# Kernel tuning notes

Hardware: AMD Instinct MI355X
Metric: run time of the kernel (lower is better)

Reference implementation:

```python
import jax, jax.numpy as jnp
import numpy as np

N = 50000
E = 600000
D_IN = 128
D_HID = 128
D_OUT = 40
BN_EPS = 1e-5


def setup_inputs() -> dict:
    key = jax.random.key(0)
    ks = jax.random.split(key, 16)
    g = lambda k, *s: (jax.random.normal(k, s, jnp.float32) * 0.05)
    return {
        "x": jax.random.normal(ks[0], (N, D_IN), jnp.float32),
        "edge_index": jax.random.randint(ks[1], (2, E), 0, N, dtype=jnp.int64),
        "W0": g(ks[2], D_IN, D_HID), "b0": jnp.zeros((D_HID,), jnp.float32),
        "W1": g(ks[3], D_HID, D_HID), "b1": jnp.zeros((D_HID,), jnp.float32),
        "W2": g(ks[4], D_HID, D_OUT), "b2": jnp.zeros((D_OUT,), jnp.float32),
        "g0": 1.0 + g(ks[5], D_HID), "be0": g(ks[6], D_HID),
        "m0": g(ks[7], D_HID), "v0": 0.5 + jax.random.uniform(ks[8], (D_HID,), jnp.float32),
        "g1": 1.0 + g(ks[9], D_HID), "be1": g(ks[10], D_HID),
        "m1": g(ks[11], D_HID), "v1": 0.5 + jax.random.uniform(ks[12], (D_HID,), jnp.float32),
    }


def reference(x, edge_index, W0, b0, W1, b1, W2, b2,
              g0, be0, m0, v0, g1, be1, m1, v1):
    n = x.shape[0]
    loop = jnp.arange(n, dtype=edge_index.dtype)
    # GCN with self-loops: A_hat = A + I, symmetric normalization
    src = jnp.concatenate([edge_index[0], loop])
    dst = jnp.concatenate([edge_index[1], loop])
    deg = jax.ops.segment_sum(jnp.ones_like(dst, jnp.float32), dst, num_segments=n)
    dinv = jax.lax.rsqrt(jnp.maximum(deg, 1.0))
    norm = dinv[src] * dinv[dst]  # [E+N]

    def conv(h, W, b):
        h = h @ W + b                                   # [N, d_out]
        msg = norm[:, None] * h[src]                    # gather + scale
        return jax.ops.segment_sum(msg, dst, num_segments=n)

    def bn_relu(h, g, be, m, v):
        return jax.nn.relu((h - m) * (g * jax.lax.rsqrt(v + BN_EPS)) + be)

    h = bn_relu(conv(x, W0, b0), g0, be0, m0, v0)
    h = bn_relu(conv(h, W1, b1), g1, be1, m1, v1)
    h = conv(h, W2, b2)
    return jax.nn.log_softmax(h, axis=-1)
```

## Files before the change

kernel.cpp:

```cpp
#include <hip/hip_runtime.h>
#include <math.h>

#define BN_EPS 1e-5f
#define CAP 96

typedef unsigned short ushort_t;
typedef __attribute__((ext_vector_type(8))) short short8;
typedef __attribute__((ext_vector_type(4))) float floatx4;

__device__ inline ushort_t f2b(float f) {
    unsigned u = __float_as_uint(f);
    unsigned r = u + 0x7FFFu + ((u >> 16) & 1u);
    return (ushort_t)(r >> 16);
}
__device__ inline float b2f(ushort_t b) { return __uint_as_float(((unsigned)b) << 16); }
__device__ inline float2 u2f2(unsigned u) {
    return make_float2(b2f((ushort_t)(u & 0xffffu)), b2f((ushort_t)(u >> 16)));
}

__device__ inline void cast_weights(const float* __restrict__ W0, const float* __restrict__ W1,
                                    const float* __restrict__ W2, ushort_t* __restrict__ Wt0,
                                    ushort_t* __restrict__ Wt1, ushort_t* __restrict__ Wt2,
                                    int i) {
    if (i < 16384) {
        int nn = i >> 7, k = i & 127;
        Wt0[i] = f2b(W0[k * 128 + nn]);
    } else if (i < 32768) {
        int j = i - 16384;
        int nn = j >> 7, k = j & 127;
        Wt1[j] = f2b(W1[k * 128 + nn]);
    } else if (i < 40960) {
        int j = i - 32768;
        int nn = j >> 7, k = j & 127;
        Wt2[j] = (nn < 40) ? f2b(W2[k * 40 + nn]) : (ushort_t)0;
    }
}

__global__ __launch_bounds__(256) void k_fill_cast(
    const int* __restrict__ ei, int* __restrict__ cnt, ushort_t* __restrict__ ell,
    const float* __restrict__ W0, const float* __restrict__ W1, const float* __restrict__ W2,
    ushort_t* __restrict__ Wt0, ushort_t* __restrict__ Wt1, ushort_t* __restrict__ Wt2,
    int E, int FB)
{
    int bid = blockIdx.x;
    if (bid < FB) {
        int e = bid * 256 + threadIdx.x;
        if (e < E) {
            int s = ei[e];
            int d = ei[E + e];
            int p = atomicAdd(&cnt[d], 1);
            if (p < CAP) ell[(size_t)d * CAP + p] = (ushort_t)s;
        }
        return;
    }
    cast_weights(W0, W1, W2, Wt0, Wt1, Wt2, (bid - FB) * 256 + threadIdx.x);
}

template<int NT, bool AF32>
__global__ __launch_bounds__(256) void k_gemm(const void* __restrict__ Av,
                                              const ushort_t* __restrict__ Wt,
                                              const float* __restrict__ bias,
                                              const int* __restrict__ cnt,
                                              ushort_t* __restrict__ C,
                                              int M, int ncols) {
    __shared__ ushort_t Ws[NT * 128];
    const int tid = threadIdx.x;
    const int ntiles = (M + 127) >> 7;
    const int wave = tid >> 6, lane = tid & 63;
    const int m = lane & 15, quad = lane >> 4;
    constexpr int CT = NT / 16;
    const int r0 = wave * 32;

    for (int t = blockIdx.x; t < ntiles; t += gridDim.x) {
        const int rbase = t << 7;
#pragma unroll
        for (int p = 0; p < NT / 16; ++p) {
            int cid = p * 256 + tid;
            int nr = cid >> 4, seg = cid & 15;
            *(uint4*)(Ws + nr * 128 + ((seg ^ (nr & 15)) << 3)) =
                *(const uint4*)(Wt + (size_t)cid * 8);
        }
        __syncthreads();

        floatx4 acc[2][CT];
#pragma unroll
        for (int rt = 0; rt < 2; ++rt)
#pragma unroll
            for (int ct = 0; ct < CT; ++ct) acc[rt][ct] = (floatx4){0.f, 0.f, 0.f, 0.f};

        const int ra = rbase + r0 + m;
        const int rb = ra + 16;
        const bool oka = ra < M, okb = rb < M;

#pragma unroll
        for (int ks = 0; ks < 4; ++ks) {
            int ko = ks * 32 + quad * 8;
            short8 a0 = {0, 0, 0, 0, 0, 0, 0, 0}, a1 = a0;
            if (AF32) {
                const float* A32 = (const float*)Av;
                if (oka) {
                    const float* p = A32 + (size_t)ra * 128 + ko;
                    float4 f0 = *(const float4*)p, f1 = *(const float4*)(p + 4);
                    a0[0] = f2b(f0.x); a0[1] = f2b(f0.y); a0[2] = f2b(f0.z); a0[3] = f2b(f0.w);
                    a0[4] = f2b(f1.x); a0[5] = f2b(f1.y); a0[6] = f2b(f1.z); a0[7] = f2b(f1.w);
                }
                if (okb) {
                    const float* p = A32 + (size_t)rb * 128 + ko;
                    float4 f0 = *(const float4*)p, f1 = *(const float4*)(p + 4);
                    a1[0] = f2b(f0.x); a1[1] = f2b(f0.y); a1[2] = f2b(f0.z); a1[3] = f2b(f0.w);
                    a1[4] = f2b(f1.x); a1[5] = f2b(f1.y); a1[6] = f2b(f1.z); a1[7] = f2b(f1.w);
                }
            } else {
                const ushort_t* A16 = (const ushort_t*)Av;
                if (oka) a0 = *(const short8*)(A16 + (size_t)ra * 128 + ko);
                if (okb) a1 = *(const short8*)(A16 + (size_t)rb * 128 + ko);
            }
#pragma unroll
            for (int ct = 0; ct < CT; ++ct) {
                short8 b = *(const short8*)(Ws + (ct * 16 + m) * 128 + (((ks * 4 + quad) ^ m) << 3));
                acc[0][ct] = __builtin_amdgcn_mfma_f32_16x16x32_bf16(a0, b, acc[0][ct], 0, 0, 0);
                acc[1][ct] = __builtin_amdgcn_mfma_f32_16x16x32_bf16(a1, b, acc[1][ct], 0, 0, 0);
            }
        }

        float dsc[2][4];
#pragma unroll
        for (int rt = 0; rt < 2; ++rt)
#pragma unroll
            for (int r = 0; r < 4; ++r) {
                int gr = rbase + r0 + rt * 16 + quad * 4 + r;
                dsc[rt][r] = (gr < M) ? rsqrtf((float)(cnt[gr] + 1)) : 0.f;
            }

        __syncthreads();
        constexpr int SEGN = NT / 8, CMASK = SEGN - 1;
#pragma unroll
        for (int rt = 0; rt < 2; ++rt)
#pragma unroll
            for (int ct = 0; ct < CT; ++ct) {
                int col = ct * 16 + m;
                float bv = (col < ncols) ? bias[col] : 0.f;
                int seg = col >> 3, cl = col & 7;
#pragma unroll
                for (int r = 0; r < 4; ++r) {
                    int row = r0 + rt * 16 + quad * 4 + r;
                    Ws[row * NT + ((seg ^ (row & CMASK)) << 3) + cl] =
                        f2b((acc[rt][ct][r] + bv) * dsc[rt][r]);
                }
            }
        __syncthreads();
        constexpr int CPT = (128 * SEGN) / 256;
#pragma unroll
        for (int p = 0; p < CPT; ++p) {
            int cid = p * 256 + tid;
            int row = cid / SEGN, seg = cid & CMASK;
            int gr = rbase + row;
            if (gr < M)
                *(uint4*)(C + (size_t)gr * NT + seg * 8) =
                    *(const uint4*)(Ws + row * NT + ((seg ^ (row & CMASK)) << 3));
        }
        __syncthreads();
    }
}

template<int NT>
__global__ __launch_bounds__(512) void fused_ag(
    const ushort_t* __restrict__ h,
    const int* __restrict__ cnt,
    const ushort_t* __restrict__ ell,
    const float* __restrict__ g, const float* __restrict__ be,
    const float* __restrict__ mB, const float* __restrict__ v,
    const ushort_t* __restrict__ Wt,
    const float* __restrict__ bias,
    ushort_t* __restrict__ C,
    int M, int ncols)
{
    __shared__ ushort_t As[16 * 128];
    __shared__ ushort_t Ws[NT * 128];
    const int tid = threadIdx.x;
    const int ntiles = (M + 15) >> 4;
    const int wave = tid >> 6, lane = tid & 63;
    const int m = lane & 15, quad = lane >> 4;
    constexpr int CT = NT / 16;
    const unsigned* h2 = (const unsigned*)h;
    unsigned* As2 = (unsigned*)As;

    const int c0 = lane * 2;
    const float s0f = g[c0] * rsqrtf(v[c0] + BN_EPS);
    const float s1f = g[c0 + 1] * rsqrtf(v[c0 + 1] + BN_EPS);
    const float m0v = mB[c0], m1v = mB[c0 + 1], b0v = be[c0], b1v = be[c0 + 1];

    for (int t = blockIdx.x; t < ntiles; t += gridDim.x) {
        const int rbase = t << 4;

        for (int cid = tid; cid < NT * 16; cid += 512) {
            int nr = cid >> 4, seg = cid & 15;
            *(uint4*)(Ws + nr * 128 + ((seg ^ (nr & 15)) << 3)) =
                *(const uint4*)(Wt + (size_t)cid * 8);
        }

#pragma unroll
        for (int rr = 0; rr < 2; ++rr) {
            const int rl = wave * 2 + rr;
            const int gr = rbase + rl;
            unsigned ov = 0;
            if (gr < M) {
                int cd = cnt[gr];
                float dv = rsqrtf((float)(cd + 1));
                float2 hv = u2f2(h2[(size_t)gr * 64 + lane]);
                float ax = hv.x, ay = hv.y;
                int c = min(cd, CAP);
                const uint4* rowv = (const uint4*)(ell + (size_t)gr * CAP);
                int k = 0;
                for (; k + 8 <= c; k += 8) {
                    uint4 iv = rowv[k >> 3];
                    int s[8] = {(int)(iv.x & 0xffffu), (int)(iv.x >> 16),
                                (int)(iv.y & 0xffffu), (int)(iv.y >> 16),
                                (int)(iv.z & 0xffffu), (int)(iv.z >> 16),
                                (int)(iv.w & 0xffffu), (int)(iv.w >> 16)};
#pragma unroll
                    for (int j = 0; j < 8; ++j) {
                        float2 tt = u2f2(h2[(size_t)s[j] * 64 + lane]);
                        ax += tt.x;
                        ay += tt.y;
                    }
                }
                if (k < c) {
                    int rem = c - k;
                    uint4 iv = rowv[k >> 3];
                    int sr[8] = {(int)(iv.x & 0xffffu), (int)(iv.x >> 16),
                                 (int)(iv.y & 0xffffu), (int)(iv.y >> 16),
                                 (int)(iv.z & 0xffffu), (int)(iv.z >> 16),
                                 (int)(iv.w & 0xffffu), (int)(iv.w >> 16)};
                    int s[8];
#pragma unroll
                    for (int j = 0; j < 8; ++j) s[j] = (j < rem) ? sr[j] : 0;
#pragma unroll
                    for (int j = 0; j < 8; ++j) {
                        float2 tt = u2f2(h2[(size_t)s[j] * 64 + lane]);
                        ax += (j < rem) ? tt.x : 0.f;
                        ay += (j < rem) ? tt.y : 0.f;
                    }
                }
                ax *= dv;
                ay *= dv;
                float o0 = fmaxf(fmaf(ax - m0v, s0f, b0v), 0.f);
                float o1 = fmaxf(fmaf(ay - m1v, s1f, b1v), 0.f);
                ov = (unsigned)f2b(o0) | ((unsigned)f2b(o1) << 16);
            }
            As2[rl * 64 + (((lane >> 2) ^ rl) << 2) + (lane & 3)] = ov;
        }
        __syncthreads();

        floatx4 acc = (floatx4){0.f, 0.f, 0.f, 0.f};
        if (wave < CT) {
#pragma unroll
            for (int ks = 0; ks < 4; ++ks) {
                short8 a0 = *(const short8*)(As + m * 128 + (((ks * 4 + quad) ^ m) << 3));
                short8 b = *(const short8*)(Ws + (wave * 16 + m) * 128 + (((ks * 4 + quad) ^ m) << 3));
                acc = __builtin_amdgcn_mfma_f32_16x16x32_bf16(a0, b, acc, 0, 0, 0);
            }
        }

        float dsc[4];
#pragma unroll
        for (int r = 0; r < 4; ++r) {
            int gr2 = rbase + quad * 4 + r;
            dsc[r] = (gr2 < M) ? rsqrtf((float)(cnt[gr2] + 1)) : 0.f;
        }

        __syncthreads();
        constexpr int SEGN = NT / 8, CMASK = SEGN - 1;
        if (wave < CT) {
            int col = wave * 16 + m;
            float bv = (col < ncols) ? bias[col] : 0.f;
            int seg = col >> 3, cl = col & 7;
#pragma unroll
            for (int r = 0; r < 4; ++r) {
                int row = quad * 4 + r;
                As[row * NT + ((seg ^ (row & CMASK)) << 3) + cl] =
                    f2b((acc[r] + bv) * dsc[r]);
            }
        }
        __syncthreads();
        for (int cid = tid; cid < 16 * SEGN; cid += 512) {
            int row = cid / SEGN, seg = cid & CMASK;
            int gr = rbase + row;
            if (gr < M)
                *(uint4*)(C + (size_t)gr * NT + seg * 8) =
                    *(const uint4*)(As + row * NT + ((seg ^ (row & CMASK)) << 3));
        }
        __syncthreads();
    }
}

__global__ __launch_bounds__(256) void k_agg40(const ushort_t* __restrict__ h,
                                               const int* __restrict__ cnt,
                                               const ushort_t* __restrict__ ell,
                                               float* __restrict__ out, int n) {
    int wv = __builtin_amdgcn_readfirstlane((blockIdx.x * 256 + threadIdx.x) >> 6);
    int lane = threadIdx.x & 63;
    if (wv >= n) return;
    int cd = cnt[wv];
    float dv = rsqrtf((float)(cd + 1));
    float acc = b2f(h[(size_t)wv * 64 + lane]);
    int c = min(cd, CAP);
    const ushort_t* row = ell + (size_t)wv * CAP;
    int k = 0;
    for (; k + 8 <= c; k += 8) {
        int s[8];
#pragma unroll
        for (int j = 0; j < 8; ++j) s[j] = row[k + j];
#pragma unroll
        for (int j = 0; j < 8; ++j) acc += b2f(h[(size_t)s[j] * 64 + lane]);
    }
    if (k < c) {
        int rem = c - k;
        int s[8];
#pragma unroll
        for (int j = 0; j < 8; ++j) {
            int sr = row[k + j];
            s[j] = (j < rem) ? sr : 0;
        }
#pragma unroll
        for (int j = 0; j < 8; ++j) {
            float t = b2f(h[(size_t)s[j] * 64 + lane]);
            acc += (j < rem) ? t : 0.f;
        }
    }
    acc *= dv;
    bool act = lane < 40;
    float xv = act ? acc : -INFINITY;
    float mx = xv;
#pragma unroll
    for (int off = 32; off > 0; off >>= 1) mx = fmaxf(mx, __shfl_xor(mx, off, 64));
    float ex = act ? expf(acc - mx) : 0.f;
    float se = ex;
#pragma unroll
    for (int off = 32; off > 0; off >>= 1) se += __shfl_xor(se, off, 64);
    float r = acc - mx - logf(se);
    if (act) out[(size_t)wv * 40 + lane] = r;
}


extern "C" void kernel_launch(void* const* d_in, const int* in_sizes, int n_in,
                              void* d_out, int out_size, void* d_ws, size_t ws_size,
                              hipStream_t stream) {
    const float* x = (const float*)d_in[0];
    const int* ei = (const int*)d_in[1];
    const float* W0 = (const float*)d_in[2];
    const float* b0 = (const float*)d_in[3];
    const float* W1 = (const float*)d_in[4];
    const float* b1 = (const float*)d_in[5];
    const float* W2 = (const float*)d_in[6];
    const float* b2 = (const float*)d_in[7];
    const float* g0 = (const float*)d_in[8];
    const float* be0 = (const float*)d_in[9];
    const float* m0 = (const float*)d_in[10];
    const float* v0 = (const float*)d_in[11];
    const float* g1 = (const float*)d_in[12];
    const float* be1 = (const float*)d_in[13];
    const float* m1 = (const float*)d_in[14];
    const float* v1 = (const float*)d_in[15];
    float* out = (float*)d_out;

    const int N = in_sizes[0] / 128;
    const int E = in_sizes[1] / 2;

    char* wp = (char*)d_ws;
    auto alloc = [&](size_t bytes) -> char* {
        char* p = wp;
        wp += (bytes + 255) & ~(size_t)255;
        return p;
    };
    int* cnt = (int*)alloc((size_t)N * 4);
    ushort_t* ell = (ushort_t*)alloc(((size_t)N * CAP + 16) * 2);
    ushort_t* hA = (ushort_t*)alloc((size_t)N * 128 * 2);
    ushort_t* hA2 = (ushort_t*)alloc((size_t)N * 128 * 2);
    ushort_t* hL = (ushort_t*)alloc((size_t)N * 64 * 2);
    ushort_t* Wt0 = (ushort_t*)alloc(128 * 128 * 2);
    ushort_t* Wt1 = (ushort_t*)alloc(128 * 128 * 2);
    ushort_t* Wt2 = (ushort_t*)alloc(64 * 128 * 2);

    const int GB = (N + 127) / 128;
    const int TG = (N + 15) / 16;
    const int FB = (E + 255) / 256;
    const int CB = 160;

    hipMemsetAsync(cnt, 0, (size_t)N * 4, stream);
    k_fill_cast<<<FB + CB, 256, 0, stream>>>(ei, cnt, ell, W0, W1, W2,
                                             Wt0, Wt1, Wt2, E, FB);
    k_gemm<128, true><<<GB, 256, 0, stream>>>(x, Wt0, b0, cnt, hA, N, 128);
    fused_ag<128><<<TG, 512, 0, stream>>>(hA, cnt, ell, g0, be0, m0, v0,
                                          Wt1, b1, hA2, N, 128);
    fused_ag<64><<<TG, 512, 0, stream>>>(hA2, cnt, ell, g1, be1, m1, v1,
                                         Wt2, b2, hL, N, 40);
    k_agg40<<<(N + 3) / 4, 256, 0, stream>>>(hL, cnt, ell, out, N);
}
```

Baseline: 235.8 us.

## Split fused aggregate+GEMM into column-sliced aggregation and separate GEMM kernels

Replaces the fused aggregation+MFMA kernel with a standalone aggregation kernel. It assigns each 16-lane group to one row and one 32-column slice, spreading gathers over four times as many blocks. The following GEMM runs through the existing k_gemm kernel. This aims to raise parallelism and drop the per-tile weight reload and LDS syncs of the fused kernel. The cost is two extra launches and a round trip of intermediate activations through global memory, and each lane group now reloads the ELL indices four times.

```diff
diff --git a/kernel.cpp b/kernel.cpp
--- a/kernel.cpp
+++ b/kernel.cpp
@@ -163,135 +163,72 @@
     }
 }
 
-template<int NT>
-__global__ __launch_bounds__(512) void fused_ag(
+__global__ __launch_bounds__(256) void agg128_sliced(
     const ushort_t* __restrict__ h,
     const int* __restrict__ cnt,
     const ushort_t* __restrict__ ell,
     const float* __restrict__ g, const float* __restrict__ be,
     const float* __restrict__ mB, const float* __restrict__ v,
-    const ushort_t* __restrict__ Wt,
-    const float* __restrict__ bias,
-    ushort_t* __restrict__ C,
-    int M, int ncols)
+    ushort_t* __restrict__ out, int n)
 {
-    __shared__ ushort_t As[16 * 128];
-    __shared__ ushort_t Ws[NT * 128];
+    const int bid = blockIdx.x;
+    const int slice = bid & 3;
     const int tid = threadIdx.x;
-    const int ntiles = (M + 15) >> 4;
     const int wave = tid >> 6, lane = tid & 63;
-    const int m = lane & 15, quad = lane >> 4;
-    constexpr int CT = NT / 16;
+    const int quad = lane >> 4, l16 = lane & 15;
+    const int r = ((bid >> 2) << 4) + wave * 4 + quad;
+    if (r >= n) return;
+    const int so = slice << 4;
     const unsigned* h2 = (const unsigned*)h;
-    unsigned* As2 = (unsigned*)As;
-
-    const int c0 = lane * 2;
+
+    const int c0 = (slice << 5) + l16 * 2;
     const float s0f = g[c0] * rsqrtf(v[c0] + BN_EPS);
     const float s1f = g[c0 + 1] * rsqrtf(v[c0 + 1] + BN_EPS);
     const float m0v = mB[c0], m1v = mB[c0 + 1], b0v = be[c0], b1v = be[c0 + 1];
 
-    for (int t = blockIdx.x; t < ntiles; t += gridDim.x) {
-        const int rbase = t << 4;
-
-        for (int cid = tid; cid < NT * 16; cid += 512) {
-            int nr = cid >> 4, seg = cid & 15;
-            *(uint4*)(Ws + nr * 128 + ((seg ^ (nr & 15)) << 3)) =
-                *(const uint4*)(Wt + (size_t)cid * 8);
-        }
-
-#pragma unroll
-        for (int rr = 0; rr < 2; ++rr) {
-            const int rl = wave * 2 + rr;
-            const int gr = rbase + rl;
-            unsigned ov = 0;
-            if (gr < M) {
-                int cd = cnt[gr];
-                float dv = rsqrtf((float)(cd + 1));
-                float2 hv = u2f2(h2[(size_t)gr * 64 + lane]);
-                float ax = hv.x, ay = hv.y;
-                int c = min(cd, CAP);
-                const uint4* rowv = (const uint4*)(ell + (size_t)gr * CAP);
-                int k = 0;
-                for (; k + 8 <= c; k += 8) {
-                    uint4 iv = rowv[k >> 3];
-                    int s[8] = {(int)(iv.x & 0xffffu), (int)(iv.x >> 16),
-                                (int)(iv.y & 0xffffu), (int)(iv.y >> 16),
-                                (int)(iv.z & 0xffffu), (int)(iv.z >> 16),
-                                (int)(iv.w & 0xffffu), (int)(iv.w >> 16)};
-#pragma unroll
-                    for (int j = 0; j < 8; ++j) {
-                        float2 tt = u2f2(h2[(size_t)s[j] * 64 + lane]);
-                        ax += tt.x;
-                        ay += tt.y;
-                    }
-                }
-                if (k < c) {
-                    int rem = c - k;
-                    uint4 iv = rowv[k >> 3];
-                    int sr[8] = {(int)(iv.x & 0xffffu), (int)(iv.x >> 16),
-                                 (int)(iv.y & 0xffffu), (int)(iv.y >> 16),
-                                 (int)(iv.z & 0xffffu), (int)(iv.z >> 16),
-                                 (int)(iv.w & 0xffffu), (int)(iv.w >> 16)};
-                    int s[8];
-#pragma unroll
-                    for (int j = 0; j < 8; ++j) s[j] = (j < rem) ? sr[j] : 0;
-#pragma unroll
-                    for (int j = 0; j < 8; ++j) {
-                        float2 tt = u2f2(h2[(size_t)s[j] * 64 + lane]);
-                        ax += (j < rem) ? tt.x : 0.f;
-                        ay += (j < rem) ? tt.y : 0.f;
-                    }
-                }
-                ax *= dv;
-                ay *= dv;
-                float o0 = fmaxf(fmaf(ax - m0v, s0f, b0v), 0.f);
-                float o1 = fmaxf(fmaf(ay - m1v, s1f, b1v), 0.f);
-                ov = (unsigned)f2b(o0) | ((unsigned)f2b(o1) << 16);
-            }
-            As2[rl * 64 + (((lane >> 2) ^ rl) << 2) + (lane & 3)] = ov;
-        }
-        __syncthreads();
-
-        floatx4 acc = (floatx4){0.f, 0.f, 0.f, 0.f};
-        if (wave < CT) {
-#pragma unroll
-            for (int ks = 0; ks < 4; ++ks) {
-                short8 a0 = *(const short8*)(As + m * 128 + (((ks * 4 + quad) ^ m) << 3));
-                short8 b = *(const short8*)(Ws + (wave * 16 + m) * 128 + (((ks * 4 + quad) ^ m) << 3));
-                acc = __builtin_amdgcn_mfma_f32_16x16x32_bf16(a0, b, acc, 0, 0, 0);
-            }
-        }
-
-        float dsc[4];
-#pragma unroll
-        for (int r = 0; r < 4; ++r) {
-            int gr2 = rbase + quad * 4 + r;
-            dsc[r] = (gr2 < M) ? rsqrtf((float)(cnt[gr2] + 1)) : 0.f;
-        }
-
-        __syncthreads();
-        constexpr int SEGN = NT / 8, CMASK = SEGN - 1;
-        if (wave < CT) {
-            int col = wave * 16 + m;
-            float bv = (col < ncols) ? bias[col] : 0.f;
-            int seg = col >> 3, cl = col & 7;
-#pragma unroll
-            for (int r = 0; r < 4; ++r) {
-                int row = quad * 4 + r;
-                As[row * NT + ((seg ^ (row & CMASK)) << 3) + cl] =
-                    f2b((acc[r] + bv) * dsc[r]);
-            }
-        }
-        __syncthreads();
-        for (int cid = tid; cid < 16 * SEGN; cid += 512) {
-            int row = cid / SEGN, seg = cid & CMASK;
-            int gr = rbase + row;
-            if (gr < M)
-                *(uint4*)(C + (size_t)gr * NT + seg * 8) =
-                    *(const uint4*)(As + row * NT + ((seg ^ (row & CMASK)) << 3));
-        }
-        __syncthreads();
-    }
+    int cd = cnt[r];
+    float dv = rsqrtf((float)(cd + 1));
+    float2 hv = u2f2(h2[(size_t)r * 64 + so + l16]);
+    float ax = hv.x, ay = hv.y;
+    int c = min(cd, CAP);
+    const ushort_t* row = ell + (size_t)r * CAP;
+    int k = 0;
+    for (; k + 8 <= c; k += 8) {
+        uint4 iv = *(const uint4*)(row + k);
+        int s[8] = {(int)(iv.x & 0xffffu), (int)(iv.x >> 16),
+                    (int)(iv.y & 0xffffu), (int)(iv.y >> 16),
+                    (int)(iv.z & 0xffffu), (int)(iv.z >> 16),
+                    (int)(iv.w & 0xffffu), (int)(iv.w >> 16)};
+#pragma unroll
+        for (int j = 0; j < 8; ++j) {
+            float2 t = u2f2(h2[(size_t)s[j] * 64 + so + l16]);
+            ax += t.x;
+            ay += t.y;
+        }
+    }
+    if (k < c) {
+        int rem = c - k;
+        uint4 iv = *(const uint4*)(row + k);
+        int sr[8] = {(int)(iv.x & 0xffffu), (int)(iv.x >> 16),
+                     (int)(iv.y & 0xffffu), (int)(iv.y >> 16),
+                     (int)(iv.z & 0xffffu), (int)(iv.z >> 16),
+                     (int)(iv.w & 0xffffu), (int)(iv.w >> 16)};
+        int s[8];
+#pragma unroll
+        for (int j = 0; j < 8; ++j) s[j] = (j < rem) ? sr[j] : 0;
+#pragma unroll
+        for (int j = 0; j < 8; ++j) {
+            float2 t = u2f2(h2[(size_t)s[j] * 64 + so + l16]);
+            ax += (j < rem) ? t.x : 0.f;
+            ay += (j < rem) ? t.y : 0.f;
+        }
+    }
+    ax *= dv;
+    ay *= dv;
+    float o0 = fmaxf(fmaf(ax - m0v, s0f, b0v), 0.f);
+    float o1 = fmaxf(fmaf(ay - m1v, s1f, b1v), 0.f);
+    unsigned ov = (unsigned)f2b(o0) | ((unsigned)f2b(o1) << 16);
+    ((unsigned*)out)[(size_t)r * 64 + so + l16] = ov;
 }
 
 __global__ __launch_bounds__(256) void k_agg40(const ushort_t* __restrict__ h,
@@ -376,14 +313,16 @@
     int* cnt = (int*)alloc((size_t)N * 4);
     ushort_t* ell = (ushort_t*)alloc(((size_t)N * CAP + 16) * 2);
     ushort_t* hA = (ushort_t*)alloc((size_t)N * 128 * 2);
+    ushort_t* hB = (ushort_t*)alloc((size_t)N * 128 * 2);
     ushort_t* hA2 = (ushort_t*)alloc((size_t)N * 128 * 2);
+    ushort_t* hB2 = (ushort_t*)alloc((size_t)N * 128 * 2);
     ushort_t* hL = (ushort_t*)alloc((size_t)N * 64 * 2);
     ushort_t* Wt0 = (ushort_t*)alloc(128 * 128 * 2);
     ushort_t* Wt1 = (ushort_t*)alloc(128 * 128 * 2);
     ushort_t* Wt2 = (ushort_t*)alloc(64 * 128 * 2);
 
     const int GB = (N + 127) / 128;
-    const int TG = (N + 15) / 16;
+    const int AG = 4 * ((N + 15) / 16);
     const int FB = (E + 255) / 256;
     const int CB = 160;
 
@@ -391,9 +330,9 @@
     k_fill_cast<<<FB + CB, 256, 0, stream>>>(ei, cnt, ell, W0, W1, W2,
                                              Wt0, Wt1, Wt2, E, FB);
     k_gemm<128, true><<<GB, 256, 0, stream>>>(x, Wt0, b0, cnt, hA, N, 128);
-    fused_ag<128><<<TG, 512, 0, stream>>>(hA, cnt, ell, g0, be0, m0, v0,
-                                          Wt1, b1, hA2, N, 128);
-    fused_ag<64><<<TG, 512, 0, stream>>>(hA2, cnt, ell, g1, be1, m1, v1,
-                                         Wt2, b2, hL, N, 40);
+    agg128_sliced<<<AG, 256, 0, stream>>>(hA, cnt, ell, g0, be0, m0, v0, hB, N);
+    k_gemm<128, false><<<GB, 256, 0, stream>>>(hB, Wt1, b1, cnt, hA2, N, 128);
+    agg128_sliced<<<AG, 256, 0, stream>>>(hA2, cnt, ell, g1, be1, m1, v1, hB2, N);
+    k_gemm<64, false><<<GB, 256, 0, stream>>>(hB2, Wt2, b2, cnt, hL, N, 40);
     k_agg40<<<(N + 3) / 4, 256, 0, stream>>>(hL, cnt, ell, out, N);
 }
```

Result: slower. 252.3 us (+7.0%).
